# Performance work log

Hardware: AMD Instinct MI355X
Metric: run time of the kernel (lower is better)

Reference implementation:

```python
import jax, jax.numpy as jnp
import numpy as np

H = 1024
V = 50000
E_SOUND, E_NUM = 40, 5
D_SOUND, D_NUM = 32, 32
IN_DIM = H + D_SOUND + D_NUM  # GRU input size
B, L = 128, 128


def setup_inputs() -> dict:
    key = jax.random.key(0)
    ks = jax.random.split(key, 16)
    s = lambda k, shape: jax.random.normal(k, shape, jnp.float32) * 0.02
    return {
        "input_seq": jax.random.randint(ks[0], (B,), 0, V),
        "last_hidden": jax.random.normal(ks[1], (1, B, H), jnp.float32),
        "encoder_outputs": jax.random.normal(ks[2], (L, B, H), jnp.float32),
        "char2num": jax.random.randint(ks[3], (V,), 0, E_NUM),
        "char2final": jax.random.randint(ks[4], (V,), 0, E_SOUND),
        "emb": s(ks[5], (V, H)),
        "sound_emb": s(ks[6], (E_SOUND, D_SOUND)),
        "num_emb": s(ks[7], (E_NUM, D_NUM)),
        "W_ih": s(ks[8], (3 * H, IN_DIM)),
        "W_hh": s(ks[9], (3 * H, H)),
        "b_ih": jnp.zeros((3 * H,), jnp.float32),
        "b_hh": jnp.zeros((3 * H,), jnp.float32),
        "W_attn": s(ks[10], (H, H)),
        "b_attn": jnp.zeros((H,), jnp.float32),
        "W_cat": s(ks[11], (H, 2 * H)),
        "b_cat": jnp.zeros((H,), jnp.float32),
        "W_out": s(ks[12], (V, H)),
        "b_out": jnp.zeros((V,), jnp.float32),
    }


def _gru_cell(x, h, W_ih, W_hh, b_ih, b_hh):
    # PyTorch GRU gate order: r, z, n
    gi = x @ W_ih.T + b_ih
    gh = h @ W_hh.T + b_hh
    i_r, i_z, i_n = jnp.split(gi, 3, axis=-1)
    h_r, h_z, h_n = jnp.split(gh, 3, axis=-1)
    r = jax.nn.sigmoid(i_r + h_r)
    z = jax.nn.sigmoid(i_z + h_z)
    n = jnp.tanh(i_n + r * h_n)
    return (1.0 - z) * n + z * h


def reference(input_seq, last_hidden, encoder_outputs, char2num, char2final,
              emb, sound_emb, num_emb, W_ih, W_hh, b_ih, b_hh,
              W_attn, b_attn, W_cat, b_cat, W_out, b_out):
    # Embeddings (eval mode -> dropout is identity)
    e = emb[input_seq]                             # [B,H]
    num_ids = char2num[input_seq]                  # [B]
    snd_ids = char2final[input_seq]                # [B]
    x = jnp.concatenate([e, sound_emb[snd_ids], num_emb[num_ids]], -1)  # [B,IN_DIM]

    # Single-step single-layer GRU
    h_new = _gru_cell(x, last_hidden[0], W_ih, W_hh, b_ih, b_hh)  # [B,H]
    hidden = h_new[None]                            # [1,B,H]
    rnn_output = h_new                              # [B,H]

    # Luong 'general' attention, batched (replaces the nested-loop .mm calls)
    proj = jnp.einsum('lbh,kh->lbk', encoder_outputs, W_attn) + b_attn  # [L,B,H]
    energies = jnp.einsum('bh,lbh->bl', rnn_output, proj)               # [B,L]
    attn_weights = jax.nn.softmax(energies, axis=1)[:, None, :]         # [B,1,L]
    context = jnp.einsum('bl,lbh->bh', attn_weights[:, 0], encoder_outputs)

    concat_out = jnp.tanh(jnp.concatenate([rnn_output, context], -1) @ W_cat.T + b_cat)
    output = concat_out @ W_out.T + b_out           # [B,V]
    return output, hidden, attn_weights
```

## Files before the change

### kernel.cpp

```cpp
#include <hip/hip_runtime.h>
#include <hip/hip_bf16.h>
#include <cstddef>

#define B_   128
#define L_   128
#define H_   1024
#define V_   50000
#define INDIM 1088

typedef short short8 __attribute__((ext_vector_type(8)));
typedef unsigned short ushort8 __attribute__((ext_vector_type(8)));
typedef unsigned short ushort4v __attribute__((ext_vector_type(4)));
typedef float f32x4 __attribute__((ext_vector_type(4)));

static __device__ __forceinline__ unsigned short f2bf(float f) {
    unsigned u = __builtin_bit_cast(unsigned, f);
    u = u + 0x7FFFu + ((u >> 16) & 1u);
    return (unsigned short)(u >> 16);
}
static __device__ __forceinline__ float bf2f(unsigned short h) {
    unsigned u = ((unsigned)h) << 16;
    return __builtin_bit_cast(float, u);
}
static __device__ __forceinline__ float sigm(float v) {
    return 1.f / (1.f + __expf(-v));
}

__global__ __launch_bounds__(256) void prep_kernel(
    const int* __restrict__ seq, const int* __restrict__ c2n,
    const int* __restrict__ c2f, const float* __restrict__ emb,
    const float* __restrict__ semb, const float* __restrict__ nemb,
    const float* __restrict__ lh,
    unsigned short* __restrict__ x_hi, unsigned short* __restrict__ x_lo,
    unsigned short* __restrict__ h_hi, unsigned short* __restrict__ h_lo)
{
    const int b = blockIdx.x, t = threadIdx.x;
    const int idx = seq[b];
    for (int i = t; i < 528; i += 256) {
        float4 v;
        unsigned short *dh, *dl;
        int off;
        if (i < 272) {
            if (i < 256) {
                v = *(const float4*)&emb[(size_t)idx * H_ + i * 4];
            } else {
                const int j = i - 256;
                if (j < 8) v = *(const float4*)&semb[c2f[idx] * 32 + j * 4];
                else       v = *(const float4*)&nemb[c2n[idx] * 32 + (j - 8) * 4];
            }
            dh = x_hi + (size_t)b * INDIM; dl = x_lo + (size_t)b * INDIM; off = i * 4;
        } else {
            const int j = i - 272;
            v = *(const float4*)&lh[(size_t)b * H_ + j * 4];
            dh = h_hi + (size_t)b * H_; dl = h_lo + (size_t)b * H_; off = j * 4;
        }
        const float fv[4] = {v.x, v.y, v.z, v.w};
        ushort4v hh, ll;
#pragma unroll
        for (int e = 0; e < 4; e++) {
            hh[e] = f2bf(fv[e]);
            ll[e] = f2bf(fv[e] - bf2f(hh[e]));
        }
        *(ushort4v*)&dh[off] = hh;
        *(ushort4v*)&dl[off] = ll;
    }
}

template<bool WT, bool SPLIT, bool TANH>
static __device__ __forceinline__ void sgemm_body(
    const unsigned short* __restrict__ Ah, const unsigned short* __restrict__ Al, int lda,
    const float* __restrict__ W, int ldw,
    const float* __restrict__ bias,
    float* __restrict__ C, int ldc, size_t pstride,
    int N, int k_len0, int k_lenB)
{
    extern __shared__ char smem_raw[];
    typedef unsigned short RowT[72];
    RowT* As_h = (RowT*)(smem_raw);
    RowT* Ws_h = (RowT*)(smem_raw + 18432);
    RowT* As_l = (RowT*)(smem_raw + 27648);
    RowT* Ws_l = (RowT*)(smem_raw + 46080);

    const int t    = threadIdx.x;
    const int lane = t & 63;
    const int wv   = t >> 6;
    const int wr   = wv >> 1;
    const int wc   = wv & 1;
    const int n0   = blockIdx.x * 64;
    const int l15  = lane & 15;
    const int g    = lane >> 4;

    const int y     = blockIdx.y;
    const int k_off = (y == 0) ? 0 : k_len0 + (y - 1) * k_lenB;
    const int k_len = (y == 0) ? k_len0 : k_lenB;
    float* Cp = C + (size_t)y * pstride;

    const int ar = t >> 3;
    const int ac = (t & 7) * 8;
    const int wn = t >> 2, wq = t & 3;
    const int nk = t >> 4, nn4 = (t & 15) * 4;

    f32x4 acc[4][2];
#pragma unroll
    for (int i = 0; i < 4; i++)
#pragma unroll
        for (int j = 0; j < 2; j++) acc[i][j] = (f32x4){0.f, 0.f, 0.f, 0.f};

#define LOAD_A(K0, RA, RAL) do {                                               \
    _Pragma("unroll")                                                          \
    for (int i_ = 0; i_ < 4; i_++)                                             \
        RA[i_] = *(const ushort8*)&Ah[(size_t)(ar + i_ * 32) * lda + (K0) + ac]; \
    if constexpr (SPLIT) {                                                     \
        _Pragma("unroll")                                                      \
        for (int i_ = 0; i_ < 4; i_++)                                         \
            RAL[i_] = *(const ushort8*)&Al[(size_t)(ar + i_ * 32) * lda + (K0) + ac]; \
    }                                                                          \
} while (0)

#define LOAD_W(K0, RW) do {                                                    \
    if constexpr (WT) {                                                        \
        const bool ok_ = (n0 + wn) < N;                                        \
        const float* wb_ = W + (size_t)(n0 + wn) * ldw + (K0);                 \
        _Pragma("unroll")                                                      \
        for (int j_ = 0; j_ < 4; j_++)                                         \
            RW[j_] = ok_ ? *(const float4*)&wb_[j_ * 16 + wq * 4]              \
                         : make_float4(0.f, 0.f, 0.f, 0.f);                    \
    } else {                                                                   \
        _Pragma("unroll")                                                      \
        for (int j_ = 0; j_ < 4; j_++)                                         \
            RW[j_] = *(const float4*)&W[(size_t)((K0) + nk + j_ * 16) * ldw + n0 + nn4]; \
    }                                                                          \
} while (0)

#define STAGE_REGS(RA, RAL, RW) do {                                           \
    _Pragma("unroll")                                                          \
    for (int i_ = 0; i_ < 4; i_++) {                                           \
        *(ushort8*)&As_h[ar + i_ * 32][ac] = RA[i_];                           \
        if constexpr (SPLIT) *(ushort8*)&As_l[ar + i_ * 32][ac] = RAL[i_];     \
    }                                                                          \
    if constexpr (WT) {                                                        \
        _Pragma("unroll")                                                      \
        for (int j_ = 0; j_ < 4; j_++) {                                       \
            const float fv_[4] = {RW[j_].x, RW[j_].y, RW[j_].z, RW[j_].w};     \
            ushort4v hh_, ll_;                                                 \
            _Pragma("unroll")                                                  \
            for (int e_ = 0; e_ < 4; e_++) {                                   \
                hh_[e_] = f2bf(fv_[e_]);                                       \
                if constexpr (SPLIT) ll_[e_] = f2bf(fv_[e_] - bf2f(hh_[e_]));  \
            }                                                                  \
            *(ushort4v*)&Ws_h[wn][j_ * 16 + wq * 4] = hh_;                     \
            if constexpr (SPLIT) *(ushort4v*)&Ws_l[wn][j_ * 16 + wq * 4] = ll_; \
        }                                                                      \
    } else {                                                                   \
        _Pragma("unroll")                                                      \
        for (int j_ = 0; j_ < 4; j_++) {                                       \
            const float fv_[4] = {RW[j_].x, RW[j_].y, RW[j_].z, RW[j_].w};     \
            _Pragma("unroll")                                                  \
            for (int e_ = 0; e_ < 4; e_++) {                                   \
                const unsigned short hb_ = f2bf(fv_[e_]);                      \
                Ws_h[nn4 + e_][nk + j_ * 16] = hb_;                            \
                if constexpr (SPLIT)                                           \
                    Ws_l[nn4 + e_][nk + j_ * 16] = f2bf(fv_[e_] - bf2f(hb_));  \
            }                                                                  \
        }                                                                      \
    }                                                                          \
} while (0)

    const int k_end = k_off + k_len;

    ushort8 ra[4], ral[4], nra[4], nral[4];
    float4 rw0[4], rw1[4], rw2[4];

    LOAD_A(k_off, ra, ral);
    LOAD_W(k_off, rw0);
    if constexpr (!SPLIT) {
        if (k_off + 64 < k_end) LOAD_W(k_off + 64, rw1);
    }

    for (int k0 = k_off; k0 < k_end; k0 += 64) {
        const bool m1 = (k0 + 64) < k_end;
        const bool m2 = (k0 + 128) < k_end;
        if (m1) {
            LOAD_A(k0 + 64, nra, nral);
            if constexpr (SPLIT) LOAD_W(k0 + 64, rw1);
        }

        STAGE_REGS(ra, ral, rw0);
        __syncthreads();

        if constexpr (!SPLIT) {
            if (m2) LOAD_W(k0 + 128, rw2);
        }

#pragma unroll
        for (int ks = 0; ks < 2; ks++) {
            const int ko = ks * 32 + g * 8;
            short8 ah[4], bh[2];
#pragma unroll
            for (int mi = 0; mi < 4; mi++)
                ah[mi] = *(const short8*)&As_h[wr * 64 + mi * 16 + l15][ko];
#pragma unroll
            for (int ni = 0; ni < 2; ni++)
                bh[ni] = *(const short8*)&Ws_h[wc * 32 + ni * 16 + l15][ko];
            if constexpr (SPLIT) {
                short8 al[4], bl[2];
#pragma unroll
                for (int mi = 0; mi < 4; mi++)
                    al[mi] = *(const short8*)&As_l[wr * 64 + mi * 16 + l15][ko];
#pragma unroll
                for (int ni = 0; ni < 2; ni++)
                    bl[ni] = *(const short8*)&Ws_l[wc * 32 + ni * 16 + l15][ko];
#pragma unroll
                for (int mi = 0; mi < 4; mi++)
#pragma unroll
                    for (int ni = 0; ni < 2; ni++) {
                        acc[mi][ni] = __builtin_amdgcn_mfma_f32_16x16x32_bf16(ah[mi], bh[ni], acc[mi][ni], 0, 0, 0);
                        acc[mi][ni] = __builtin_amdgcn_mfma_f32_16x16x32_bf16(ah[mi], bl[ni], acc[mi][ni], 0, 0, 0);
                        acc[mi][ni] = __builtin_amdgcn_mfma_f32_16x16x32_bf16(al[mi], bh[ni], acc[mi][ni], 0, 0, 0);
                    }
            } else {
#pragma unroll
                for (int mi = 0; mi < 4; mi++)
#pragma unroll
                    for (int ni = 0; ni < 2; ni++)
                        acc[mi][ni] = __builtin_amdgcn_mfma_f32_16x16x32_bf16(ah[mi], bh[ni], acc[mi][ni], 0, 0, 0);
            }
        }
        __syncthreads();

        if (m1) {
#pragma unroll
            for (int i = 0; i < 4; i++) {
                ra[i] = nra[i];
                if constexpr (SPLIT) ral[i] = nral[i];
            }
#pragma unroll
            for (int j = 0; j < 4; j++) {
                rw0[j] = rw1[j];
                if constexpr (!SPLIT) rw1[j] = rw2[j];
            }
        }
    }
#undef LOAD_A
#undef LOAD_W
#undef STAGE_REGS

#pragma unroll
    for (int mi = 0; mi < 4; mi++) {
#pragma unroll
        for (int ni = 0; ni < 2; ni++) {
            const int col = n0 + wc * 32 + ni * 16 + l15;
            if (col < N) {
                const float bb = bias ? bias[col] : 0.f;
#pragma unroll
                for (int r = 0; r < 4; r++) {
                    const int row = wr * 64 + mi * 16 + g * 4 + r;
                    float v = acc[mi][ni][r] + bb;
                    if (TANH) v = tanhf(v);
                    Cp[(size_t)row * ldc + col] = v;
                }
            }
        }
    }
}

template<bool WT, bool SPLIT, bool TANH>
__global__ __launch_bounds__(256, 2) void sgemm(
    const unsigned short* __restrict__ Ah, const unsigned short* __restrict__ Al, int lda,
    const float* __restrict__ W, int ldw,
    const float* __restrict__ bias,
    float* __restrict__ C, int ldc, size_t pstride,
    int N, int k_len0, int k_lenB)
{
    sgemm_body<WT, SPLIT, TANH>(Ah, Al, lda, W, ldw, bias, C, ldc, pstride, N, k_len0, k_lenB);
}

__global__ __launch_bounds__(256, 2) void gru_gemm(
    const unsigned short* __restrict__ x_hi,
    const float* __restrict__ W_ih,
    const unsigned short* __restrict__ h_hi,
    const float* __restrict__ W_hh,
    float* __restrict__ gi, float* __restrict__ gh)
{
    if (blockIdx.z == 0)
        sgemm_body<true, false, false>(x_hi, x_hi, INDIM, W_ih, INDIM, nullptr,
                                       gi, 3072, (size_t)128 * 3072, 3072, 320, 256);
    else
        sgemm_body<true, false, false>(h_hi, h_hi, H_, W_hh, H_, nullptr,
                                       gh, 3072, (size_t)128 * 3072, 3072, 256, 256);
}

__global__ __launch_bounds__(256, 2) void q_cat_kernel(
    const unsigned short* __restrict__ cat_hi, const unsigned short* __restrict__ cat_lo,
    const float* __restrict__ W_attn, const float* __restrict__ W_cat,
    float* __restrict__ q_part, float* __restrict__ co_part)
{
    if (blockIdx.z == 0) {
        sgemm_body<false, true, false>(cat_hi, cat_lo, 2048, W_attn, H_, nullptr,
                                       q_part, H_, (size_t)128 * 1024, H_, 256, 256);
    } else {
        if (blockIdx.y >= 2) return;
        sgemm_body<true, false, false>(cat_hi, cat_hi, 2048, W_cat, 2048, nullptr,
                                       co_part, H_, (size_t)128 * 1024, H_, 512, 512);
    }
}

__global__ __launch_bounds__(256) void gru_gates_kernel(
    const float* __restrict__ gi, const float* __restrict__ gh,
    const float* __restrict__ b_ih, const float* __restrict__ b_hh,
    const float* __restrict__ h_prev,
    float* __restrict__ hid_out,
    unsigned short* __restrict__ cat_hi, unsigned short* __restrict__ cat_lo)
{
    const int id = blockIdx.x * 256 + threadIdx.x;
    const int b = id >> 10, j = id & 1023;
    const size_t base = (size_t)b * 3072 + j;
    float ir = b_ih[j], iz = b_ih[1024 + j], in_ = b_ih[2048 + j];
    float hr = b_hh[j], hz = b_hh[1024 + j], hn = b_hh[2048 + j];
#pragma unroll
    for (int p = 0; p < 4; p++) {
        const float* gp = gi + (size_t)p * (128 * 3072);
        const float* hp = gh + (size_t)p * (128 * 3072);
        ir += gp[base]; iz += gp[base + 1024]; in_ += gp[base + 2048];
        hr += hp[base]; hz += hp[base + 1024]; hn += hp[base + 2048];
    }
    const float r = sigm(ir + hr);
    const float z = sigm(iz + hz);
    const float n = tanhf(in_ + r * hn);
    const float h = (1.f - z) * n + z * h_prev[id];
    hid_out[id] = h;
    const unsigned short hb = f2bf(h);
    cat_hi[(size_t)b * 2048 + j] = hb;
    cat_lo[(size_t)b * 2048 + j] = f2bf(h - bf2f(hb));
}

__global__ __launch_bounds__(512) void energy_partial_kernel(
    const float* __restrict__ qp, const float* __restrict__ enc,
    float* __restrict__ epart)
{
    const int s = blockIdx.x, b = blockIdx.y;
    const int t = threadIdx.x, lane = t & 63, wv = t >> 6;
    __shared__ float q_s[256];
    if (t < 256) {
        const size_t o = (size_t)b * H_ + s * 256 + t;
        q_s[t] = qp[o] + qp[o + 131072] + qp[o + 262144] + qp[o + 393216];
    }
    __syncthreads();
    const float4 qv = *(const float4*)&q_s[lane * 4];
    const float* encb = enc + (size_t)b * H_ + s * 256;
    for (int l0 = 0; l0 < 16; l0++) {
        const int l = wv * 16 + l0;
        float4 ev = *(const float4*)&encb[(size_t)l * (B_ * H_) + lane * 4];
        float p = ev.x * qv.x + ev.y * qv.y + ev.z * qv.z + ev.w * qv.w;
#pragma unroll
        for (int off = 32; off > 0; off >>= 1) p += __shfl_xor(p, off);
        if (lane == 0) epart[((size_t)b * 128 + l) * 4 + s] = p;
    }
}

__global__ __launch_bounds__(256) void context_softmax_kernel(
    const float* __restrict__ epart, const float* __restrict__ enc,
    unsigned short* __restrict__ cat_hi, float* __restrict__ attnw)
{
    const int s = blockIdx.x, b = blockIdx.y, t = threadIdx.x;
    const int lane = t & 63, wv = t >> 6;
    __shared__ float w_s[128];
    __shared__ float red[4];

    float e = -INFINITY;
    if (t < 128) {
        float4 pe = *(const float4*)&epart[((size_t)b * 128 + t) * 4];
        e = pe.x + pe.y + pe.z + pe.w;
    }
    float mx = e;
#pragma unroll
    for (int off = 32; off > 0; off >>= 1) mx = fmaxf(mx, __shfl_xor(mx, off));
    if (lane == 0) red[wv] = mx;
    __syncthreads();
    const float gm = fmaxf(fmaxf(red[0], red[1]), fmaxf(red[2], red[3]));
    __syncthreads();
    float ex = (t < 128) ? __expf(e - gm) : 0.f;
    float sm = ex;
#pragma unroll
    for (int off = 32; off > 0; off >>= 1) sm += __shfl_xor(sm, off);
    if (lane == 0) red[wv] = sm;
    __syncthreads();
    const float gs = red[0] + red[1] + red[2] + red[3];
    if (t < 128) {
        const float w = ex / gs;
        w_s[t] = w;
        if (s == 0) attnw[(size_t)b * L_ + t] = w;
    }
    __syncthreads();

    const int h = s * 256 + t;
    const float* encb = enc + (size_t)b * H_ + h;
    float c = 0.f;
#pragma unroll 4
    for (int l = 0; l < 128; l++)
        c += w_s[l] * encb[(size_t)l * (B_ * H_)];
    cat_hi[(size_t)b * 2048 + 1024 + h] = f2bf(c);
}

__global__ __launch_bounds__(256) void co_reduce_kernel(
    const float* __restrict__ co_part, const float* __restrict__ b_cat,
    unsigned short* __restrict__ co_hi)
{
    const int id = blockIdx.x * 256 + threadIdx.x;
    const int j = id & 1023;
    float s = b_cat[j];
#pragma unroll
    for (int p = 0; p < 4; p++) s += co_part[(size_t)p * 131072 + id];
    co_hi[id] = f2bf(tanhf(s));
}

extern "C" void kernel_launch(void* const* d_in, const int* in_sizes, int n_in,
                              void* d_out, int out_size, void* d_ws, size_t ws_size,
                              hipStream_t stream)
{
    const int*   seq    = (const int*)  d_in[0];
    const float* lh     = (const float*)d_in[1];
    const float* enc    = (const float*)d_in[2];
    const int*   c2n    = (const int*)  d_in[3];
    const int*   c2f    = (const int*)  d_in[4];
    const float* emb    = (const float*)d_in[5];
    const float* semb   = (const float*)d_in[6];
    const float* nemb   = (const float*)d_in[7];
    const float* W_ih   = (const float*)d_in[8];
    const float* W_hh   = (const float*)d_in[9];
    const float* b_ih   = (const float*)d_in[10];
    const float* b_hh   = (const float*)d_in[11];
    const float* W_attn = (const float*)d_in[12];
    const float* W_cat  = (const float*)d_in[14];
    const float* b_cat  = (const float*)d_in[15];
    const float* W_out  = (const float*)d_in[16];
    const float* b_out  = (const float*)d_in[17];

    float* out    = (float*)d_out;
    float* hidden = out + (size_t)B_ * V_;
    float* attnw  = hidden + (size_t)B_ * H_;

    unsigned short* x_hi   = (unsigned short*)d_ws;
    unsigned short* x_lo   = x_hi   + (size_t)128 * INDIM;
    unsigned short* h_hi   = x_lo   + (size_t)128 * INDIM;
    unsigned short* h_lo   = h_hi   + (size_t)128 * 1024;
    unsigned short* cat_hi = h_lo   + (size_t)128 * 1024;
    unsigned short* cat_lo = cat_hi + (size_t)128 * 2048;
    unsigned short* co_hi  = cat_lo + (size_t)128 * 2048;
    float* fbase   = (float*)(co_hi + (size_t)128 * 1024);
    float* gi_part = fbase;
    float* gh_part = gi_part + (size_t)4 * 128 * 3072;
    float* q_part  = fbase;
    float* co_part = q_part + (size_t)4 * 128 * 1024;
    float* epart   = co_part + (size_t)4 * 128 * 1024;

    const int SMEM_SPLIT = 55296;
    const int SMEM_PLAIN = 27648;

    hipLaunchKernelGGL(prep_kernel, dim3(B_), dim3(256), 0, stream,
                       seq, c2n, c2f, emb, semb, nemb, lh, x_hi, x_lo, h_hi, h_lo);
    hipLaunchKernelGGL(gru_gemm, dim3(48, 4, 2), dim3(256), SMEM_PLAIN, stream,
                       x_hi, W_ih, h_hi, W_hh, gi_part, gh_part);
    hipLaunchKernelGGL(gru_gates_kernel, dim3(512), dim3(256), 0, stream,
                       gi_part, gh_part, b_ih, b_hh, lh, hidden, cat_hi, cat_lo);
    hipLaunchKernelGGL(q_cat_kernel, dim3(16, 4, 2), dim3(256), SMEM_SPLIT, stream,
                       cat_hi, cat_lo, W_attn, W_cat, q_part, co_part);
    hipLaunchKernelGGL(energy_partial_kernel, dim3(4, 128), dim3(512), 0, stream,
                       q_part, enc, epart);
    hipLaunchKernelGGL(context_softmax_kernel, dim3(4, 128), dim3(256), 0, stream,
                       epart, enc, cat_hi, attnw);
    hipLaunchKernelGGL((sgemm<true, false, false>), dim3(16, 2), dim3(256), SMEM_PLAIN, stream,
                       cat_hi + 1024, cat_hi + 1024, 2048, W_cat + 1024, 2048,
                       (const float*)nullptr,
                       co_part + (size_t)2 * 128 * 1024, H_, (size_t)128 * 1024,
                       H_, 512, 512);
    hipLaunchKernelGGL(co_reduce_kernel, dim3(512), dim3(256), 0, stream,
                       co_part, b_cat, co_hi);
    hipLaunchKernelGGL((sgemm<true, false, false>), dim3((V_ + 63) / 64, 1), dim3(256), SMEM_PLAIN, stream,
                       co_hi, co_hi, H_, W_out, H_, b_out,
                       out, V_, (size_t)0, V_, H_, H_);
}
```

Baseline: 154.8 us.

## Replace output projection sgemm with dedicated 16-row MFMA kernel

The final vocab projection (128x50000x1024) now runs in a new kernel instead of the generic sgemm. Each block loads 16 full rows of W_out at once, converts them to bf16 in shared memory with a packed hardware convert, and computes all 128 batch rows, with activations read straight from global memory. This gives 3125 small blocks for more parallelism and removes the K-loop staging of the generic GEMM, making the kernel a single streaming pass over W_out. In exchange, A is re-read from L2 by every block and each block holds many float4 registers.

```diff
diff --git a/kernel.cpp b/kernel.cpp
--- a/kernel.cpp
+++ b/kernel.cpp
@@ -25,6 +25,13 @@
 static __device__ __forceinline__ float sigm(float v) {
     return 1.f / (1.f + __expf(-v));
 }
+static __device__ __forceinline__ unsigned cvt_pk(float lo, float hi) {
+    unsigned r;
+    asm("v_cvt_pk_bf16_f32 %0, %1, %2" : "=v"(r) : "v"(lo), "v"(hi));
+    return r;
+}
+
+#define MFMA16(a, b, c) __builtin_amdgcn_mfma_f32_16x16x32_bf16((a), (b), (c), 0, 0, 0)
 
 __global__ __launch_bounds__(256) void prep_kernel(
     const int* __restrict__ seq, const int* __restrict__ c2n,
@@ -214,16 +221,16 @@
                 for (int mi = 0; mi < 4; mi++)
 #pragma unroll
                     for (int ni = 0; ni < 2; ni++) {
-                        acc[mi][ni] = __builtin_amdgcn_mfma_f32_16x16x32_bf16(ah[mi], bh[ni], acc[mi][ni], 0, 0, 0);
-                        acc[mi][ni] = __builtin_amdgcn_mfma_f32_16x16x32_bf16(ah[mi], bl[ni], acc[mi][ni], 0, 0, 0);
-                        acc[mi][ni] = __builtin_amdgcn_mfma_f32_16x16x32_bf16(al[mi], bh[ni], acc[mi][ni], 0, 0, 0);
+                        acc[mi][ni] = MFMA16(ah[mi], bh[ni], acc[mi][ni]);
+                        acc[mi][ni] = MFMA16(ah[mi], bl[ni], acc[mi][ni]);
+                        acc[mi][ni] = MFMA16(al[mi], bh[ni], acc[mi][ni]);
                     }
             } else {
 #pragma unroll
                 for (int mi = 0; mi < 4; mi++)
 #pragma unroll
                     for (int ni = 0; ni < 2; ni++)
-                        acc[mi][ni] = __builtin_amdgcn_mfma_f32_16x16x32_bf16(ah[mi], bh[ni], acc[mi][ni], 0, 0, 0);
+                        acc[mi][ni] = MFMA16(ah[mi], bh[ni], acc[mi][ni]);
             }
         }
         __syncthreads();
@@ -412,6 +419,58 @@
 #pragma unroll
     for (int p = 0; p < 4; p++) s += co_part[(size_t)p * 131072 + id];
     co_hi[id] = f2bf(tanhf(s));
+}
+
+__global__ __launch_bounds__(256, 4) void out_rows_kernel(
+    const unsigned short* __restrict__ co_hi,
+    const float* __restrict__ W_out,
+    const float* __restrict__ b_out,
+    float* __restrict__ C)
+{
+    __shared__ unsigned short Ws[16][1032];
+    const int t = threadIdx.x;
+    const int lane = t & 63;
+    const int wv = t >> 6;
+    const int l15 = lane & 15, g = lane >> 4;
+    const int n0 = blockIdx.x * 16;
+    const float* wt = W_out + (size_t)n0 * H_;
+
+    float4 wreg[16];
+#pragma unroll
+    for (int i = 0; i < 16; i++)
+        wreg[i] = *(const float4*)&wt[(size_t)i * H_ + t * 4];
+#pragma unroll
+    for (int i = 0; i < 16; i++) {
+        const unsigned p01 = cvt_pk(wreg[i].x, wreg[i].y);
+        const unsigned p23 = cvt_pk(wreg[i].z, wreg[i].w);
+        ushort4v hh;
+        hh[0] = (unsigned short)p01; hh[1] = (unsigned short)(p01 >> 16);
+        hh[2] = (unsigned short)p23; hh[3] = (unsigned short)(p23 >> 16);
+        *(ushort4v*)&Ws[i][t * 4] = hh;
+    }
+    __syncthreads();
+
+    f32x4 acc0 = (f32x4){0.f, 0.f, 0.f, 0.f};
+    f32x4 acc1 = (f32x4){0.f, 0.f, 0.f, 0.f};
+    const unsigned short* a0 = co_hi + (size_t)(wv * 32 + l15) * H_ + g * 8;
+    const unsigned short* a1 = a0 + (size_t)16 * H_;
+
+#pragma unroll 4
+    for (int ks = 0; ks < 32; ks++) {
+        const short8 bh  = *(const short8*)&Ws[l15][ks * 32 + g * 8];
+        const short8 ah0 = *(const short8*)&a0[ks * 32];
+        const short8 ah1 = *(const short8*)&a1[ks * 32];
+        acc0 = MFMA16(ah0, bh, acc0);
+        acc1 = MFMA16(ah1, bh, acc1);
+    }
+
+    const int col = n0 + l15;
+    const float bb = b_out[col];
+#pragma unroll
+    for (int r = 0; r < 4; r++) {
+        C[(size_t)(wv * 32 + g * 4 + r) * V_ + col]      = acc0[r] + bb;
+        C[(size_t)(wv * 32 + 16 + g * 4 + r) * V_ + col] = acc1[r] + bb;
+    }
 }
 
 extern "C" void kernel_launch(void* const* d_in, const int* in_sizes, int n_in,
@@ -476,7 +535,6 @@
                        H_, 512, 512);
     hipLaunchKernelGGL(co_reduce_kernel, dim3(512), dim3(256), 0, stream,
                        co_part, b_cat, co_hi);
-    hipLaunchKernelGGL((sgemm<true, false, false>), dim3((V_ + 63) / 64, 1), dim3(256), SMEM_PLAIN, stream,
-                       co_hi, co_hi, H_, W_out, H_, b_out,
-                       out, V_, (size_t)0, V_, H_, H_);
-}
+    hipLaunchKernelGGL(out_rows_kernel, dim3(V_ / 16), dim3(256), 0, stream,
+                       co_hi, W_out, b_out, out);
+}
```

New measurement: 204.6 us. 1.32x slower.
